# Kernel optimization log

Measured on AMD Instinct MI355X. Metric: run time of the kernel, lower is better.

The kernel has to match this reference:

```python
import jax, jax.numpy as jnp
import numpy as np

S = 512          # sentence length
WE, PE = 300, 100  # word / pos embedding dims
H = 512          # lstm hidden per direction
M = 512          # mlp hidden
VW, VP = 50000, 45


def _lstm_dir(x, w_ih, w_hh, b, reverse):
    # x: [S, in], w_ih: [4H, in], w_hh: [4H, H], b: [4H]; PyTorch gate order i,f,g,o
    Hd = w_hh.shape[1]
    xg = x @ w_ih.T + b  # precompute input contribution [S, 4H]
    def step(carry, gx):
        h, c = carry
        g = gx + h @ w_hh.T
        i, f, gg, o = jnp.split(g, 4)
        i = jax.nn.sigmoid(i); f = jax.nn.sigmoid(f)
        gg = jnp.tanh(gg); o = jax.nn.sigmoid(o)
        c = f * c + i * gg
        h = o * jnp.tanh(c)
        return (h, c), h
    init = (jnp.zeros((Hd,), x.dtype), jnp.zeros((Hd,), x.dtype))
    _, hs = jax.lax.scan(step, init, xg, reverse=reverse)
    return hs  # [S, H]


def _bilstm_layer(x, w_ih, w_hh, b_ih, b_hh):
    # stacked direction axis 0: [2, 4H, in], [2, 4H, H], [2, 4H]
    b = b_ih + b_hh
    fwd = _lstm_dir(x, w_ih[0], w_hh[0], b[0], False)
    bwd = _lstm_dir(x, w_ih[1], w_hh[1], b[1], True)
    return jnp.concatenate([fwd, bwd], axis=-1)  # [S, 2H]


def setup_inputs() -> dict:
    key = jax.random.key(0)
    ks = jax.random.split(key, 20)
    sc = 0.1
    inp = {
        'word_idx': jax.random.randint(ks[0], (S,), 0, VW),
        'pos_idx': jax.random.randint(ks[1], (S,), 0, VP),
        'heads': jax.random.randint(ks[2], (S,), 0, S),
        'word_emb': jax.random.normal(ks[3], (VW, WE), jnp.float32) * sc,
        'pos_emb': jax.random.normal(ks[4], (VP, PE), jnp.float32) * sc,
        # layer 0 bi-LSTM, input dim WE+PE=400
        'w_ih0': jax.random.normal(ks[5], (2, 4 * H, WE + PE), jnp.float32) * sc,
        'w_hh0': jax.random.normal(ks[6], (2, 4 * H, H), jnp.float32) * sc,
        'b_ih0': jax.random.normal(ks[7], (2, 4 * H), jnp.float32) * sc,
        'b_hh0': jax.random.normal(ks[8], (2, 4 * H), jnp.float32) * sc,
        # layer 1 bi-LSTM, input dim 2H=1024
        'w_ih1': jax.random.normal(ks[9], (2, 4 * H, 2 * H), jnp.float32) * sc,
        'w_hh1': jax.random.normal(ks[10], (2, 4 * H, H), jnp.float32) * sc,
        'b_ih1': jax.random.normal(ks[11], (2, 4 * H), jnp.float32) * sc,
        'b_hh1': jax.random.normal(ks[12], (2, 4 * H), jnp.float32) * sc,
        # edge scorer MLP: Linear(4H, M) -> tanh -> Linear(M, 1)
        'W1': jax.random.normal(ks[13], (M, 4 * H), jnp.float32) * (1.0 / np.sqrt(4 * H)),
        'b1': jax.random.normal(ks[14], (M,), jnp.float32) * sc,
        'W2': jax.random.normal(ks[15], (M,), jnp.float32) * (1.0 / np.sqrt(M)),
        'b2': jax.random.normal(ks[16], (), jnp.float32) * sc,
    }
    return inp


def reference(word_idx, pos_idx, heads, word_emb, pos_emb,
              w_ih0, w_hh0, b_ih0, b_hh0, w_ih1, w_hh1, b_ih1, b_hh1,
              W1, b1, W2, b2):
    x = jnp.concatenate([word_emb[word_idx], pos_emb[pos_idx]], axis=1)  # [S, 400]
    h = _bilstm_layer(x, w_ih0, w_hh0, b_ih0, b_hh0)  # [S, 2H]
    h = _bilstm_layer(h, w_ih1, w_hh1, b_ih1, b_hh1)  # [S, 2H]
    twoH = h.shape[1]
    # cat(h_head, h_mod) @ W1.T == h_head @ A.T + h_mod @ B.T
    A, B = W1[:, :twoH], W1[:, twoH:]
    Xh = h @ A.T  # [S, M] head contribution
    Ym = h @ B.T  # [S, M] modifier contribution
    hid = jnp.tanh(Xh[:, None, :] + Ym[None, :, :] + b1)  # [S, S, M]; [head, modifier]
    scores = hid @ W2 + b2  # [S, S]
    # NLLLOSS: -mean_m log( exp(s[head_m, m]) / sum_h exp(s[h, m]) )
    lsm = jax.nn.log_softmax(scores, axis=0)
    loss = -jnp.mean(lsm[heads, jnp.arange(heads.shape[0])])
    return loss
```

## Files before the change

kernel.cpp:

```cpp
#include <hip/hip_runtime.h>
#include <hip/hip_bf16.h>

#define REC_NWG 32

__device__ __forceinline__ float sigm_(float x) { return 1.f / (1.f + __expf(-x)); }
__device__ __forceinline__ float tanh_(float x) { return 1.f - 2.f / (__expf(2.f * x) + 1.f); }

__global__ void embed_kernel(const int* __restrict__ wi, const int* __restrict__ pi,
                             const float* __restrict__ we, const float* __restrict__ pe,
                             float* __restrict__ x) {
    int t = blockIdx.x;
    int w = wi[t], p = pi[t];
    for (int c = threadIdx.x; c < 400; c += 128) {
        x[t * 400 + c] = (c < 300) ? we[(size_t)w * 300 + c] : pe[(size_t)p * 100 + (c - 300)];
    }
}

__global__ __launch_bounds__(256) void gemm_xwt(
    const float* __restrict__ X, int ldx,
    const float* __restrict__ W, int ldw, size_t wbs,
    const float* __restrict__ b1, const float* __restrict__ b2, int bbs,
    float* __restrict__ C, int ldc, size_t cbs, int K) {
    int z = blockIdx.z;
    const float* Wz = W + (size_t)z * wbs;
    float* Cz = C + (size_t)z * cbs;
    int n0 = blockIdx.x * 64, m0 = blockIdx.y * 64;
    int tid = threadIdx.x;
    __shared__ __align__(16) float Xs[16][68];
    __shared__ __align__(16) float Ws[16][68];
    int lr = tid >> 2;
    int lk = (tid & 3) * 4;
    int ty = tid >> 4, tx = tid & 15;
    float acc[4][4] = {{0.f}};
    const float* Xp = X + (size_t)(m0 + lr) * ldx + lk;
    const float* Wp = Wz + (size_t)(n0 + lr) * ldw + lk;
    for (int k0 = 0; k0 < K; k0 += 16) {
        float4 xv = *(const float4*)(Xp + k0);
        float4 wv = *(const float4*)(Wp + k0);
        __syncthreads();
        Xs[lk + 0][lr] = xv.x; Xs[lk + 1][lr] = xv.y; Xs[lk + 2][lr] = xv.z; Xs[lk + 3][lr] = xv.w;
        Ws[lk + 0][lr] = wv.x; Ws[lk + 1][lr] = wv.y; Ws[lk + 2][lr] = wv.z; Ws[lk + 3][lr] = wv.w;
        __syncthreads();
#pragma unroll
        for (int kk = 0; kk < 16; ++kk) {
            float4 a = *(const float4*)&Xs[kk][ty * 4];
            float4 b = *(const float4*)&Ws[kk][tx * 4];
            acc[0][0] += a.x * b.x; acc[0][1] += a.x * b.y; acc[0][2] += a.x * b.z; acc[0][3] += a.x * b.w;
            acc[1][0] += a.y * b.x; acc[1][1] += a.y * b.y; acc[1][2] += a.y * b.z; acc[1][3] += a.y * b.w;
            acc[2][0] += a.z * b.x; acc[2][1] += a.z * b.y; acc[2][2] += a.z * b.z; acc[2][3] += a.z * b.w;
            acc[3][0] += a.w * b.x; acc[3][1] += a.w * b.y; acc[3][2] += a.w * b.z; acc[3][3] += a.w * b.w;
        }
    }
#pragma unroll
    for (int i = 0; i < 4; ++i) {
        int m = m0 + ty * 4 + i;
#pragma unroll
        for (int j = 0; j < 4; ++j) {
            int n = n0 + tx * 4 + j;
            float bv = 0.f;
            if (b1) bv += b1[z * bbs + n];
            if (b2) bv += b2[z * bbs + n];
            Cz[(size_t)m * ldc + n] = acc[i][j] + bv;
        }
    }
}

__global__ __launch_bounds__(256, 1) void lstm_rec(
    const float* __restrict__ xg, const float* __restrict__ w_hh,
    float* __restrict__ hs, int* __restrict__ flags) {
    int bid = blockIdx.x;
    int d = bid >> 5;
    int k = bid & 31;
    int tid = threadIdx.x;
    int r = tid >> 2;
    int q = tid & 3;
    int j_local = r >> 2;
    int gate = r & 3;
    int grow = gate * 512 + k * 16 + j_local;

    const float* wrow = w_hh + (size_t)d * 2048 * 512 + (size_t)grow * 512 + q * 128;
    float w[128];
#pragma unroll
    for (int i = 0; i < 32; ++i) {
        float4 v = ((const float4*)wrow)[i];
        w[4 * i + 0] = v.x; w[4 * i + 1] = v.y; w[4 * i + 2] = v.z; w[4 * i + 3] = v.w;
    }
    const float* xgd = xg + (size_t)d * 512 * 2048;
    int* cnt = flags + d * 512;

    __shared__ float4 h4[128];
    __shared__ float gate_lds[64];
    float c = 0.f;

    for (int ti = 0; ti < 512; ++ti) {
        int t = d ? (511 - ti) : ti;
        float a0 = 0.f, a1 = 0.f, a2 = 0.f, a3 = 0.f;
        if (ti > 0) {
            int tp = d ? (t + 1) : (t - 1);
            if (tid == 0) {
                while (__hip_atomic_load(&cnt[ti - 1], __ATOMIC_ACQUIRE, __HIP_MEMORY_SCOPE_AGENT) < REC_NWG) {
                    __builtin_amdgcn_s_sleep(8);
                }
            }
            __syncthreads();
            if (tid < 128) {
                float4 v = ((const float4*)(hs + (size_t)tp * 1024 + d * 512))[tid];
                h4[tid ^ (tid >> 5)] = v;
            }
            __syncthreads();
#pragma unroll
            for (int i = 0; i < 32; ++i) {
                float4 hv = h4[(q * 32 + i) ^ q];
                a0 += w[4 * i + 0] * hv.x;
                a1 += w[4 * i + 1] * hv.y;
                a2 += w[4 * i + 2] * hv.z;
                a3 += w[4 * i + 3] * hv.w;
            }
        }
        float acc = (a0 + a1) + (a2 + a3);
        acc += __shfl_xor(acc, 1);
        acc += __shfl_xor(acc, 2);
        if (q == 0) gate_lds[r] = acc + xgd[(size_t)t * 2048 + grow];
        __syncthreads();
        if (tid < 16) {
            float gi = gate_lds[4 * tid + 0];
            float gf = gate_lds[4 * tid + 1];
            float gg = gate_lds[4 * tid + 2];
            float go = gate_lds[4 * tid + 3];
            float iv = sigm_(gi), fv = sigm_(gf), gv = tanh_(gg), ov = sigm_(go);
            c = fv * c + iv * gv;
            float h = ov * tanh_(c);
            hs[(size_t)t * 1024 + d * 512 + k * 16 + tid] = h;
        }
        __syncthreads();
        if (tid == 0) {
            __hip_atomic_fetch_add(&cnt[ti], 1, __ATOMIC_RELEASE, __HIP_MEMORY_SCOPE_AGENT);
        }
    }
}

__global__ __launch_bounds__(256) void scorer(const float* __restrict__ Xh, const float* __restrict__ Ym,
                                              const float* __restrict__ W2, float* __restrict__ sc) {
    int i0 = blockIdx.y * 16, j0 = blockIdx.x * 16;
    int tid = threadIdx.x;
    __shared__ float xs[512][16];
    __shared__ float ys[512][16];
    __shared__ float w2s[512];
    {
        int rr = tid >> 4, cc = (tid & 15) * 32;
        const float4* xg4 = (const float4*)(Xh + (size_t)(i0 + rr) * 512 + cc);
        const float4* yg4 = (const float4*)(Ym + (size_t)(j0 + rr) * 512 + cc);
#pragma unroll
        for (int u = 0; u < 8; ++u) {
            float4 a = xg4[u];
            float4 b = yg4[u];
            int mb = cc + u * 4;
            xs[mb + 0][rr] = a.x; xs[mb + 1][rr] = a.y; xs[mb + 2][rr] = a.z; xs[mb + 3][rr] = a.w;
            ys[mb + 0][rr] = b.x; ys[mb + 1][rr] = b.y; ys[mb + 2][rr] = b.z; ys[mb + 3][rr] = b.w;
        }
        for (int m = tid; m < 512; m += 256) w2s[m] = W2[m];
    }
    __syncthreads();
    int ii = tid >> 4, jj = tid & 15;
    float acc = 0.f;
#pragma unroll 4
    for (int m = 0; m < 512; ++m) {
        float v = xs[m][ii] + ys[m][jj];
        acc += w2s[m] * (1.f - 2.f / (__expf(2.f * v) + 1.f));
    }
    sc[(size_t)(i0 + ii) * 512 + (j0 + jj)] = acc;
}

__global__ __launch_bounds__(256) void col_lse(const float* __restrict__ sc, const int* __restrict__ heads,
                                               float* __restrict__ part) {
    int j = blockIdx.x;
    int tid = threadIdx.x;
    float v1 = sc[(size_t)tid * 512 + j];
    float v2 = sc[(size_t)(tid + 256) * 512 + j];
    float m = fmaxf(v1, v2);
    for (int o = 1; o < 64; o <<= 1) m = fmaxf(m, __shfl_xor(m, o));
    __shared__ float red[4], red2[4];
    if ((tid & 63) == 0) red[tid >> 6] = m;
    __syncthreads();
    m = fmaxf(fmaxf(red[0], red[1]), fmaxf(red[2], red[3]));
    float s = __expf(v1 - m) + __expf(v2 - m);
    for (int o = 1; o < 64; o <<= 1) s += __shfl_xor(s, o);
    if ((tid & 63) == 0) red2[tid >> 6] = s;
    __syncthreads();
    if (tid == 0) {
        s = red2[0] + red2[1] + red2[2] + red2[3];
        part[j] = sc[(size_t)heads[j] * 512 + j] - (m + logf(s));
    }
}

__global__ void final_red(const float* __restrict__ part, float* __restrict__ out) {
    int tid = threadIdx.x;
    float v = part[tid];
    for (int o = 1; o < 64; o <<= 1) v += __shfl_xor(v, o);
    __shared__ float red[8];
    if ((tid & 63) == 0) red[tid >> 6] = v;
    __syncthreads();
    if (tid == 0) {
        float s = 0.f;
        for (int i = 0; i < 8; ++i) s += red[i];
        out[0] = -s / 512.f;
    }
}

extern "C" void kernel_launch(void* const* d_in, const int* in_sizes, int n_in,
                              void* d_out, int out_size, void* d_ws, size_t ws_size,
                              hipStream_t stream) {
    const int* word_idx = (const int*)d_in[0];
    const int* pos_idx  = (const int*)d_in[1];
    const int* heads    = (const int*)d_in[2];
    const float* we     = (const float*)d_in[3];
    const float* pe     = (const float*)d_in[4];
    const float* w_ih0  = (const float*)d_in[5];
    const float* w_hh0  = (const float*)d_in[6];
    const float* b_ih0  = (const float*)d_in[7];
    const float* b_hh0  = (const float*)d_in[8];
    const float* w_ih1  = (const float*)d_in[9];
    const float* w_hh1  = (const float*)d_in[10];
    const float* b_ih1  = (const float*)d_in[11];
    const float* b_hh1  = (const float*)d_in[12];
    const float* W1     = (const float*)d_in[13];
    const float* b1v    = (const float*)d_in[14];
    const float* W2     = (const float*)d_in[15];
    float* out = (float*)d_out;

    float* ws  = (float*)d_ws;
    float* x_  = ws;
    float* xg0 = x_  + 204800;
    float* hs0 = xg0 + 2097152;
    float* xg1 = hs0 + 524288;
    float* hs1 = xg1 + 2097152;
    float* Xh  = hs1 + 524288;
    float* Ym  = Xh  + 262144;
    float* scb = Ym  + 262144;
    float* part= scb + 262144;
    int*  flg  = (int*)(part + 512);

    hipMemsetAsync(flg, 0, 2048 * sizeof(int), stream);

    embed_kernel<<<512, 128, 0, stream>>>(word_idx, pos_idx, we, pe, x_);

    gemm_xwt<<<dim3(32, 8, 2), 256, 0, stream>>>(x_, 400, w_ih0, 400, (size_t)2048 * 400,
                                                 b_ih0, b_hh0, 2048, xg0, 2048, (size_t)512 * 2048, 400);
    lstm_rec<<<64, 256, 0, stream>>>(xg0, w_hh0, hs0, flg);

    gemm_xwt<<<dim3(32, 8, 2), 256, 0, stream>>>(hs0, 1024, w_ih1, 1024, (size_t)2048 * 1024,
                                                 b_ih1, b_hh1, 2048, xg1, 2048, (size_t)512 * 2048, 1024);
    lstm_rec<<<64, 256, 0, stream>>>(xg1, w_hh1, hs1, flg + 1024);

    gemm_xwt<<<dim3(8, 8, 1), 256, 0, stream>>>(hs1, 1024, W1, 2048, 0,
                                                b1v, nullptr, 0, Xh, 512, 0, 1024);
    gemm_xwt<<<dim3(8, 8, 1), 256, 0, stream>>>(hs1, 1024, W1 + 1024, 2048, 0,
                                                nullptr, nullptr, 0, Ym, 512, 0, 1024);

    scorer<<<dim3(32, 32), 256, 0, stream>>>(Xh, Ym, W2, scb);
    col_lse<<<512, 256, 0, stream>>>(scb, heads, part);
    final_red<<<1, 512, 0, stream>>>(part, out);
}
```

Baseline: 4.047 ms.

## Halve LSTM recurrence workgroups and replace shared counter with per-workgroup sequence flags

The recurrent LSTM kernel now runs 16 workgroups of 512 threads per direction instead of 32 of 256, so each group computes 32 hidden units per step. Cross-workgroup synchronisation moves from a single atomic counter per timestep to one monotonically increasing sequence number per workgroup. A full wavefront polls these numbers with a wave vote, then loads h itself. The input-gate load is issued before the wait, and the trailing block barrier is dropped. The aim is to shorten the per-step barrier latency of the serial recurrence, at the cost of more work per workgroup and tighter register pressure.

```diff
diff --git a/kernel.cpp b/kernel.cpp
--- a/kernel.cpp
+++ b/kernel.cpp
@@ -1,7 +1,7 @@
 #include <hip/hip_runtime.h>
 #include <hip/hip_bf16.h>
 
-#define REC_NWG 32
+#define RWG 16
 
 __device__ __forceinline__ float sigm_(float x) { return 1.f / (1.f + __expf(-x)); }
 __device__ __forceinline__ float tanh_(float x) { return 1.f - 2.f / (__expf(2.f * x) + 1.f); }
@@ -65,47 +65,54 @@
     }
 }
 
-__global__ __launch_bounds__(256, 1) void lstm_rec(
+__global__ __launch_bounds__(512, 2) void lstm_rec(
     const float* __restrict__ xg, const float* __restrict__ w_hh,
-    float* __restrict__ hs, int* __restrict__ flags) {
+    float* __restrict__ hs, int* __restrict__ seqs) {
     int bid = blockIdx.x;
-    int d = bid >> 5;
-    int k = bid & 31;
+    int d = bid >> 4;
+    int k = bid & 15;
     int tid = threadIdx.x;
     int r = tid >> 2;
     int q = tid & 3;
     int j_local = r >> 2;
     int gate = r & 3;
-    int grow = gate * 512 + k * 16 + j_local;
-
-    const float* wrow = w_hh + (size_t)d * 2048 * 512 + (size_t)grow * 512 + q * 128;
+    int grow = gate * 512 + k * 32 + j_local;
+
+    const float* wrow = w_hh + (size_t)d * (2048 * 512) + (size_t)grow * 512 + q * 128;
     float w[128];
 #pragma unroll
     for (int i = 0; i < 32; ++i) {
         float4 v = ((const float4*)wrow)[i];
         w[4 * i + 0] = v.x; w[4 * i + 1] = v.y; w[4 * i + 2] = v.z; w[4 * i + 3] = v.w;
     }
-    const float* xgd = xg + (size_t)d * 512 * 2048;
-    int* cnt = flags + d * 512;
+    const float* xgd = xg + (size_t)d * (512 * 2048);
+    int* sq = seqs + d * RWG;
 
     __shared__ float4 h4[128];
-    __shared__ float gate_lds[64];
+    __shared__ float gate_lds[128];
     float c = 0.f;
 
     for (int ti = 0; ti < 512; ++ti) {
         int t = d ? (511 - ti) : ti;
+        float xgv = 0.f;
+        if (q == 0) xgv = xgd[(size_t)t * 2048 + grow];
+
         float a0 = 0.f, a1 = 0.f, a2 = 0.f, a3 = 0.f;
         if (ti > 0) {
             int tp = d ? (t + 1) : (t - 1);
-            if (tid == 0) {
-                while (__hip_atomic_load(&cnt[ti - 1], __ATOMIC_ACQUIRE, __HIP_MEMORY_SCOPE_AGENT) < REC_NWG) {
-                    __builtin_amdgcn_s_sleep(8);
+            if (tid < 64) {
+                while (true) {
+                    int v = ti;
+                    if (tid < RWG) v = __hip_atomic_load(&sq[tid], __ATOMIC_ACQUIRE, __HIP_MEMORY_SCOPE_AGENT);
+                    if (__all(v >= ti)) break;
+                    __builtin_amdgcn_s_sleep(1);
                 }
-            }
-            __syncthreads();
-            if (tid < 128) {
-                float4 v = ((const float4*)(hs + (size_t)tp * 1024 + d * 512))[tid];
-                h4[tid ^ (tid >> 5)] = v;
+                __builtin_amdgcn_fence(__ATOMIC_ACQUIRE, "agent");
+                const float4* hp = (const float4*)(hs + (size_t)tp * 1024 + d * 512);
+                float4 v0 = hp[tid];
+                float4 v1 = hp[tid + 64];
+                h4[tid ^ (tid >> 5)] = v0;
+                h4[(tid + 64) ^ ((tid + 64) >> 5)] = v1;
             }
             __syncthreads();
 #pragma unroll
@@ -120,9 +127,9 @@
         float acc = (a0 + a1) + (a2 + a3);
         acc += __shfl_xor(acc, 1);
         acc += __shfl_xor(acc, 2);
-        if (q == 0) gate_lds[r] = acc + xgd[(size_t)t * 2048 + grow];
+        if (q == 0) gate_lds[r] = acc + xgv;
         __syncthreads();
-        if (tid < 16) {
+        if (tid < 32) {
             float gi = gate_lds[4 * tid + 0];
             float gf = gate_lds[4 * tid + 1];
             float gg = gate_lds[4 * tid + 2];
@@ -130,11 +137,10 @@
             float iv = sigm_(gi), fv = sigm_(gf), gv = tanh_(gg), ov = sigm_(go);
             c = fv * c + iv * gv;
             float h = ov * tanh_(c);
-            hs[(size_t)t * 1024 + d * 512 + k * 16 + tid] = h;
-        }
-        __syncthreads();
+            hs[(size_t)t * 1024 + d * 512 + k * 32 + tid] = h;
+        }
         if (tid == 0) {
-            __hip_atomic_fetch_add(&cnt[ti], 1, __ATOMIC_RELEASE, __HIP_MEMORY_SCOPE_AGENT);
+            __hip_atomic_store(&sq[k], ti + 1, __ATOMIC_RELEASE, __HIP_MEMORY_SCOPE_AGENT);
         }
     }
 }
@@ -240,17 +246,17 @@
     float* part= scb + 262144;
     int*  flg  = (int*)(part + 512);
 
-    hipMemsetAsync(flg, 0, 2048 * sizeof(int), stream);
+    hipMemsetAsync(flg, 0, 256 * sizeof(int), stream);
 
     embed_kernel<<<512, 128, 0, stream>>>(word_idx, pos_idx, we, pe, x_);
 
     gemm_xwt<<<dim3(32, 8, 2), 256, 0, stream>>>(x_, 400, w_ih0, 400, (size_t)2048 * 400,
                                                  b_ih0, b_hh0, 2048, xg0, 2048, (size_t)512 * 2048, 400);
-    lstm_rec<<<64, 256, 0, stream>>>(xg0, w_hh0, hs0, flg);
+    lstm_rec<<<32, 512, 0, stream>>>(xg0, w_hh0, hs0, flg);
 
     gemm_xwt<<<dim3(32, 8, 2), 256, 0, stream>>>(hs0, 1024, w_ih1, 1024, (size_t)2048 * 1024,
                                                  b_ih1, b_hh1, 2048, xg1, 2048, (size_t)512 * 2048, 1024);
-    lstm_rec<<<64, 256, 0, stream>>>(xg1, w_hh1, hs1, flg + 1024);
+    lstm_rec<<<32, 512, 0, stream>>>(xg1, w_hh1, hs1, flg + 32);
 
     gemm_xwt<<<dim3(8, 8, 1), 256, 0, stream>>>(hs1, 1024, W1, 2048, 0,
                                                 b1v, nullptr, 0, Xh, 512, 0, 1024);
```

After: 3.978 ms. Within noise of the previous version (-1.7%).

## Replace per-step atomic counter barrier with per-workgroup sequence flags in LSTM recurrence

Applied to the files above, without the earlier changes.

Replaces the global per-timestep atomic counter with a per-workgroup sequence array. Wave 1 publishes h and then its own flag with relaxed stores, and wave 0 polls all 32 flags in parallel and loads the next h directly into padded LDS. This removes one block-wide barrier, the serialized single-thread spin and fetch-add per step, and prefetches the xg value early to shorten the critical path of the recurrence. The risk is in memory-ordering correctness: relaxed stores plus an explicit waitcnt and a workgroup-scope acquire fence may not be enough to make cross-CU data visible.

```diff
diff --git a/kernel.cpp b/kernel.cpp
--- a/kernel.cpp
+++ b/kernel.cpp
@@ -1,7 +1,7 @@
 #include <hip/hip_runtime.h>
 #include <hip/hip_bf16.h>
 
-#define REC_NWG 32
+#define RWG 32
 
 __device__ __forceinline__ float sigm_(float x) { return 1.f / (1.f + __expf(-x)); }
 __device__ __forceinline__ float tanh_(float x) { return 1.f - 2.f / (__expf(2.f * x) + 1.f); }
@@ -67,50 +67,46 @@
 
 __global__ __launch_bounds__(256, 1) void lstm_rec(
     const float* __restrict__ xg, const float* __restrict__ w_hh,
-    float* __restrict__ hs, int* __restrict__ flags) {
+    float* __restrict__ hs, int* __restrict__ seqs) {
     int bid = blockIdx.x;
     int d = bid >> 5;
     int k = bid & 31;
     int tid = threadIdx.x;
     int r = tid >> 2;
     int q = tid & 3;
-    int j_local = r >> 2;
+    int jl = r >> 2;
     int gate = r & 3;
-    int grow = gate * 512 + k * 16 + j_local;
-
-    const float* wrow = w_hh + (size_t)d * 2048 * 512 + (size_t)grow * 512 + q * 128;
+    int grow = gate * 512 + k * 16 + jl;
+
+    const float* wrow = w_hh + (size_t)d * (2048 * 512) + (size_t)grow * 512 + q * 128;
     float w[128];
 #pragma unroll
     for (int i = 0; i < 32; ++i) {
         float4 v = ((const float4*)wrow)[i];
         w[4 * i + 0] = v.x; w[4 * i + 1] = v.y; w[4 * i + 2] = v.z; w[4 * i + 3] = v.w;
     }
-    const float* xgd = xg + (size_t)d * 512 * 2048;
-    int* cnt = flags + d * 512;
-
-    __shared__ float4 h4[128];
-    __shared__ float gate_lds[64];
+#pragma unroll
+    for (int i = 0; i < 128; ++i) asm volatile("" : "+v"(w[i]));
+
+    const float* xgd = xg + (size_t)d * (512 * 2048);
+    int* sq = seqs + d * RWG;
+    float* hsd = hs + d * 512;
+    const int wv = tid >> 6;
+    const int l = tid & 63;
+
+    __shared__ __align__(16) float h4[4 * 132];
+    __shared__ __align__(16) float gate_lds[64];
     float c = 0.f;
 
     for (int ti = 0; ti < 512; ++ti) {
         int t = d ? (511 - ti) : ti;
+        float xgv = (q == 0) ? xgd[(size_t)t * 2048 + grow] : 0.f;
+
         float a0 = 0.f, a1 = 0.f, a2 = 0.f, a3 = 0.f;
         if (ti > 0) {
-            int tp = d ? (t + 1) : (t - 1);
-            if (tid == 0) {
-                while (__hip_atomic_load(&cnt[ti - 1], __ATOMIC_ACQUIRE, __HIP_MEMORY_SCOPE_AGENT) < REC_NWG) {
-                    __builtin_amdgcn_s_sleep(8);
-                }
-            }
-            __syncthreads();
-            if (tid < 128) {
-                float4 v = ((const float4*)(hs + (size_t)tp * 1024 + d * 512))[tid];
-                h4[tid ^ (tid >> 5)] = v;
-            }
-            __syncthreads();
 #pragma unroll
             for (int i = 0; i < 32; ++i) {
-                float4 hv = h4[(q * 32 + i) ^ q];
+                float4 hv = *(const float4*)&h4[q * 132 + 4 * i];
                 a0 += w[4 * i + 0] * hv.x;
                 a1 += w[4 * i + 1] * hv.y;
                 a2 += w[4 * i + 2] * hv.z;
@@ -120,22 +116,39 @@
         float acc = (a0 + a1) + (a2 + a3);
         acc += __shfl_xor(acc, 1);
         acc += __shfl_xor(acc, 2);
-        if (q == 0) gate_lds[r] = acc + xgd[(size_t)t * 2048 + grow];
-        __syncthreads();
-        if (tid < 16) {
-            float gi = gate_lds[4 * tid + 0];
-            float gf = gate_lds[4 * tid + 1];
-            float gg = gate_lds[4 * tid + 2];
-            float go = gate_lds[4 * tid + 3];
-            float iv = sigm_(gi), fv = sigm_(gf), gv = tanh_(gg), ov = sigm_(go);
-            c = fv * c + iv * gv;
-            float h = ov * tanh_(c);
-            hs[(size_t)t * 1024 + d * 512 + k * 16 + tid] = h;
-        }
-        __syncthreads();
-        if (tid == 0) {
-            __hip_atomic_fetch_add(&cnt[ti], 1, __ATOMIC_RELEASE, __HIP_MEMORY_SCOPE_AGENT);
-        }
+        if (q == 0) gate_lds[r] = acc + xgv;
+        __syncthreads();
+
+        if (wv == 1) {
+            if (l < 16) {
+                float4 g = *(const float4*)&gate_lds[4 * l];
+                float iv = sigm_(g.x), fv = sigm_(g.y), gv = tanh_(g.z), ov = sigm_(g.w);
+                c = fv * c + iv * gv;
+                float h = ov * tanh_(c);
+                __hip_atomic_store(&hsd[(size_t)t * 1024 + k * 16 + l], h,
+                                   __ATOMIC_RELAXED, __HIP_MEMORY_SCOPE_AGENT);
+            }
+            asm volatile("s_waitcnt vmcnt(0)" ::: "memory");
+            if (l == 0) {
+                __hip_atomic_store(&sq[k], ti + 1, __ATOMIC_RELAXED, __HIP_MEMORY_SCOPE_AGENT);
+            }
+        } else if (wv == 0 && ti < 511) {
+            while (true) {
+                int v = ti + 1;
+                if (l < RWG) v = __hip_atomic_load(&sq[l], __ATOMIC_RELAXED, __HIP_MEMORY_SCOPE_AGENT);
+                if (__all(v >= ti + 1)) break;
+                __builtin_amdgcn_s_sleep(2);
+            }
+            __builtin_amdgcn_fence(__ATOMIC_ACQUIRE, "workgroup");
+            const unsigned long long* hp = (const unsigned long long*)(hsd + (size_t)t * 1024);
+#pragma unroll
+            for (int j = 0; j < 4; ++j) {
+                unsigned long long v = __hip_atomic_load(hp + j * 64 + l,
+                                                         __ATOMIC_RELAXED, __HIP_MEMORY_SCOPE_AGENT);
+                *(unsigned long long*)&h4[j * 132 + 2 * l] = v;
+            }
+        }
+        __syncthreads();
     }
 }
 
@@ -240,7 +253,7 @@
     float* part= scb + 262144;
     int*  flg  = (int*)(part + 512);
 
-    hipMemsetAsync(flg, 0, 2048 * sizeof(int), stream);
+    hipMemsetAsync(flg, 0, 256 * sizeof(int), stream);
 
     embed_kernel<<<512, 128, 0, stream>>>(word_idx, pos_idx, we, pe, x_);
 
@@ -250,7 +263,7 @@
 
     gemm_xwt<<<dim3(32, 8, 2), 256, 0, stream>>>(hs0, 1024, w_ih1, 1024, (size_t)2048 * 1024,
                                                  b_ih1, b_hh1, 2048, xg1, 2048, (size_t)512 * 2048, 1024);
-    lstm_rec<<<64, 256, 0, stream>>>(xg1, w_hh1, hs1, flg + 1024);
+    lstm_rec<<<64, 256, 0, stream>>>(xg1, w_hh1, hs1, flg + 64);
 
     gemm_xwt<<<dim3(8, 8, 1), 256, 0, stream>>>(hs1, 1024, W1, 2048, 0,
                                                 b1v, nullptr, 0, Xh, 512, 0, 1024);
```

Measured after the change: 4.293 ms. 1.06x slower.
